# Optimization experiments

Hardware: AMD Instinct MI355X
Metric: run time of the kernel (lower is better)

The kernel has to match this reference:

```python
import jax, jax.numpy as jnp
import numpy as np

S, B, DIM = 1024, 4, 768
N_EXPERTS = 8
# hidden_dim = 256 * ceil(int(2*4*dim/3)/256) = 2048 for dim=768
HID = 2048


def setup_inputs() -> dict:
    key = jax.random.key(0)
    ks = jax.random.split(key, 6)
    scale = 0.02
    return {
        "hidden_states": jax.random.normal(ks[0], (S, B, DIM), dtype=jnp.float32),
        "router_w": jax.random.normal(ks[1], (DIM, N_EXPERTS), dtype=jnp.float32) * scale,
        "router_b": jnp.zeros((N_EXPERTS,), dtype=jnp.float32),
        "w1": jax.random.normal(ks[2], (N_EXPERTS, DIM, HID), dtype=jnp.float32) * scale,
        "w2": jax.random.normal(ks[3], (N_EXPERTS, DIM, HID), dtype=jnp.float32) * scale,
        "w3": jax.random.normal(ks[4], (N_EXPERTS, HID, DIM), dtype=jnp.float32) * scale,
    }


def reference(hidden_states, router_w, router_b, w1, w2, w3):
    s, b, h = hidden_states.shape
    # top-1 router
    route = jax.nn.softmax(hidden_states @ router_w + router_b, axis=2)  # [s,b,E]
    max_prob = jnp.max(route, axis=2).reshape(-1, 1)   # [T,1]
    max_ind = jnp.argmax(route, axis=2).reshape(-1)    # [T]
    x = hidden_states.reshape(-1, h)                   # [T,d]

    out = jnp.zeros_like(x)
    # fixed small loop over experts; masked dispatch (tokens not routed to e
    # are zeroed so they contribute nothing)
    for e in range(N_EXPERTS):
        mask = (max_ind == e)[:, None]                 # [T,1]
        xe = jnp.where(mask, x, 0.0)
        oe = (jax.nn.silu(xe @ w1[e]) * (xe @ w2[e])) @ w3[e]
        out = out + jnp.where(mask, oe, 0.0)

    # original stores expert outputs in a bf16 buffer before the prob combine
    out = out.astype(jnp.bfloat16) * max_prob          # bf16 * f32 -> f32
    return out.reshape(s, b, h)
```

## Files before the change

kernel.cpp:

```cpp
#include <hip/hip_runtime.h>


#define T_TOK 4096
#define DIM   768
#define HID   2048
#define NE    8
#define ECAP  1024

#define KB1 24
#define NB1 128
#define KB2 64
#define NB2 48
#define MBC 64

typedef _Float16 f16x8 __attribute__((ext_vector_type(8)));
typedef float    f32x4 __attribute__((ext_vector_type(4)));

#define AS1 __attribute__((address_space(1)))
#define AS3 __attribute__((address_space(3)))

__device__ __forceinline__ void gload_lds16(const _Float16* g, _Float16* l) {
    __builtin_amdgcn_global_load_lds((const AS1 unsigned int*)g,
                                     (AS3 unsigned int*)l, 16, 0, 0);
}

__device__ __forceinline__ float bf16_rne(float v) {
    unsigned u = __float_as_uint(v);
    unsigned r = (u + 0x7fffu + ((u >> 16) & 1u)) & 0xffff0000u;
    return __uint_as_float(r);
}

__global__ __launch_bounds__(256) void moe_convert_kernel(
    const float* __restrict__ w1, const float* __restrict__ w2,
    const float* __restrict__ w3, _Float16* __restrict__ w1s,
    _Float16* __restrict__ w2s, _Float16* __restrict__ w3s)
{
    const int bid = blockIdx.x;
    const float* src; _Float16* dst; int N, KBc, ngrp, kgrp;
    if (bid < 1536) {
        const int e = bid / 192, tile = bid % 192;
        src = w1 + (size_t)e * DIM * HID; dst = w1s + (size_t)e * NB1 * KB1 * 512;
        N = HID; KBc = KB1; ngrp = tile & 15; kgrp = tile >> 4;
    } else if (bid < 3072) {
        const int r = bid - 1536, e = r / 192, tile = r % 192;
        src = w2 + (size_t)e * DIM * HID; dst = w2s + (size_t)e * NB1 * KB1 * 512;
        N = HID; KBc = KB1; ngrp = tile & 15; kgrp = tile >> 4;
    } else {
        const int r = bid - 3072, e = r / 192, tile = r % 192;
        src = w3 + (size_t)e * HID * DIM; dst = w3s + (size_t)e * NB2 * KB2 * 512;
        N = DIM; KBc = KB2; ngrp = tile % 6; kgrp = tile / 6;
    }

    __shared__ float Lt[64 * 130];
    const int t  = threadIdx.x;
    const int c4 = (t & 31) * 4;
    const int r0 = (t >> 5) * 8;
    const float* p = src + (size_t)(kgrp * 64 + r0) * N + ngrp * 128 + c4;
    float4 v[8];
#pragma unroll
    for (int j = 0; j < 8; ++j) v[j] = *(const float4*)(p + (size_t)j * N);
#pragma unroll
    for (int j = 0; j < 8; ++j) {
        float* row = &Lt[(r0 + j) * 130 + c4];
        *(float2*)(row)     = make_float2(v[j].x, v[j].y);
        *(float2*)(row + 2) = make_float2(v[j].z, v[j].w);
    }
    __syncthreads();

    const int l = t & 63, w = t >> 6;
    const int fr = l & 15, fq = l >> 4;
#pragma unroll
    for (int i = 0; i < 4; ++i) {
        const int cell = w * 4 + i;
        const int kbl = cell >> 3, nbl = cell & 7;
        f16x8 h;
#pragma unroll
        for (int j = 0; j < 8; ++j)
            h[j] = (_Float16)Lt[(kbl * 32 + fq * 8 + j) * 130 + nbl * 16 + fr];
        const int nb = ngrp * 8 + nbl, kb = kgrp * 2 + kbl;
        *(f16x8*)(dst + ((size_t)nb * KBc + kb) * 512 + l * 8) = h;
    }
}

__global__ __launch_bounds__(256) void moe_router_kernel(
    const float* __restrict__ X, const float* __restrict__ rw,
    const float* __restrict__ rb, float* __restrict__ probs,
    int* __restrict__ maxind)
{
    const int t = blockIdx.x * 4 + (threadIdx.x >> 6);
    const int l = threadIdx.x & 63;
    const int e = l >> 3;
    const int g = l & 7;
    const float* x = X + (size_t)t * DIM + g * 96;
    const float* w = rw + e;

    double s0 = 0.0, s1 = 0.0;
#pragma unroll
    for (int j4 = 0; j4 < 24; ++j4) {
        const float4 xv = *(const float4*)(x + j4 * 4);
        const int d = (g * 96 + j4 * 4) * NE;
        s0 += (double)xv.x * (double)w[d];
        s1 += (double)xv.y * (double)w[d + NE];
        s0 += (double)xv.z * (double)w[d + 2 * NE];
        s1 += (double)xv.w * (double)w[d + 3 * NE];
    }
    double s = s0 + s1;
    s += __shfl_xor(s, 1, 64);
    s += __shfl_xor(s, 2, 64);
    s += __shfl_xor(s, 4, 64);
    s += (double)rb[e];

    double m = s; int mi = e;
#pragma unroll
    for (int o = 8; o <= 32; o <<= 1) {
        const double om = __shfl_xor(m, o, 64);
        const int   omi = __shfl_xor(mi, o, 64);
        if (om > m || (om == m && omi < mi)) { m = om; mi = omi; }
    }
    float ex = __expf((float)(s - m));
#pragma unroll
    for (int o = 8; o <= 32; o <<= 1) ex += __shfl_xor(ex, o, 64);

    if (l == 0) { probs[t] = 1.0f / ex; maxind[t] = mi; }
}

__global__ __launch_bounds__(256) void moe_lists_kernel(
    const int* __restrict__ maxind, int* __restrict__ counts,
    int* __restrict__ lists)
{
    const int e = blockIdx.x;
    const int tid = threadIdx.x, wid = tid >> 6, lane = tid & 63;
    __shared__ int wsum[4];
    int* dst = lists + e * T_TOK;
    int base = 0;
    for (int t0 = 0; t0 < T_TOK; t0 += 256) {
        const int t = t0 + tid;
        const bool pred = (maxind[t] == e);
        const unsigned long long bal = __ballot(pred);
        const int prefix = __popcll(bal & ((1ull << lane) - 1ull));
        if (lane == 0) wsum[wid] = __popcll(bal);
        __syncthreads();
        int woff = 0;
#pragma unroll
        for (int w2 = 0; w2 < 4; ++w2)
            if (w2 < wid) woff += wsum[w2];
        const int tot = wsum[0] + wsum[1] + wsum[2] + wsum[3];
        if (pred) dst[base + woff + prefix] = t;
        base += tot;
        __syncthreads();
    }
    if (tid == 0) counts[e] = base;
}

__global__ __launch_bounds__(256) void moe_gather_kernel(
    const float* __restrict__ X, const int* __restrict__ lists,
    const int* __restrict__ counts, _Float16* __restrict__ Ag)
{
    const int e = blockIdx.z;
    int cnt = counts[e]; if (cnt > ECAP) cnt = ECAP;
    const int mgrp = blockIdx.y;
    if (mgrp * 64 >= ((cnt + 63) & ~63)) return;
    const int t = threadIdx.x, w = t >> 6, l = t & 63;
    const int mb = mgrp * 4 + w;
    const int m  = mb * 16 + (l & 15);
    const bool valid = (m < cnt);
    const int tok = valid ? lists[e * T_TOK + m] : 0;
    const float* xr = X + (size_t)tok * DIM + (l >> 4) * 8;
#pragma unroll
    for (int i = 0; i < 4; ++i) {
        const int kb = blockIdx.x * 4 + i;
        float4 a = make_float4(0.f, 0.f, 0.f, 0.f), b = a;
        if (valid) {
            a = *(const float4*)(xr + kb * 32);
            b = *(const float4*)(xr + kb * 32 + 4);
        }
        f16x8 h;
        h[0] = (_Float16)a.x; h[1] = (_Float16)a.y; h[2] = (_Float16)a.z; h[3] = (_Float16)a.w;
        h[4] = (_Float16)b.x; h[5] = (_Float16)b.y; h[6] = (_Float16)b.z; h[7] = (_Float16)b.w;
        *(f16x8*)(Ag + ((size_t)(e * MBC + mb) * KB1 + kb) * 512 + l * 8) = h;
    }
}

__global__ __launch_bounds__(256, 4) void moe_gemm1_kernel(
    const _Float16* __restrict__ Ag, const _Float16* __restrict__ w1s,
    const _Float16* __restrict__ w2s, const int* __restrict__ counts,
    _Float16* __restrict__ Hs)
{
    const int e = blockIdx.z;
    int cnt = counts[e]; if (cnt > ECAP) cnt = ECAP;
    const int by = blockIdx.y, bx = blockIdx.x;
    if (by * 128 >= cnt) return;
    const int t = threadIdx.x, w = t >> 6, l = t & 63;
    const int wm = w & 1, wn = w >> 1;

    __shared__ _Float16 Ls[2][16 * 512];

    const int c0s = w * 4;
    const _Float16* gsrc[4];
#pragma unroll
    for (int i = 0; i < 4; ++i) {
        const int c = c0s + i;
        if (c < 8)
            gsrc[i] = Ag  + ((size_t)((e * MBC + by * 8 + c) * KB1)) * 512;
        else if (c < 12)
            gsrc[i] = w1s + ((size_t)((e * NB1 + bx * 4 + (c - 8)) * KB1)) * 512;
        else
            gsrc[i] = w2s + ((size_t)((e * NB1 + bx * 4 + (c - 12)) * KB1)) * 512;
        gsrc[i] += (size_t)l * 8;
    }

    f32x4 acc1[4][2], acc2[4][2];
    const f32x4 zero = {0.f, 0.f, 0.f, 0.f};
#pragma unroll
    for (int i = 0; i < 4; ++i)
#pragma unroll
        for (int j = 0; j < 2; ++j) { acc1[i][j] = zero; acc2[i][j] = zero; }

    auto STAGE = [&](int kb, _Float16* Lb) {
#pragma unroll
        for (int i = 0; i < 4; ++i)
            gload_lds16(gsrc[i] + (size_t)kb * 512, Lb + (c0s + i) * 512);
    };

    STAGE(0, &Ls[0][0]);
    __syncthreads();
    for (int kb = 0; kb < KB1; ++kb) {
        _Float16* Lb = &Ls[kb & 1][0];
        if (kb + 1 < KB1) STAGE(kb + 1, &Ls[(kb + 1) & 1][0]);

        f16x8 a[4], p[2], q[2];
#pragma unroll
        for (int i = 0; i < 4; ++i)
            a[i] = *(const f16x8*)(Lb + (wm * 4 + i) * 512 + l * 8);
#pragma unroll
        for (int j = 0; j < 2; ++j) {
            p[j] = *(const f16x8*)(Lb + (8  + wn * 2 + j) * 512 + l * 8);
            q[j] = *(const f16x8*)(Lb + (12 + wn * 2 + j) * 512 + l * 8);
        }
#pragma unroll
        for (int i = 0; i < 4; ++i)
#pragma unroll
            for (int j = 0; j < 2; ++j) {
                acc1[i][j] = __builtin_amdgcn_mfma_f32_16x16x32_f16(a[i], p[j], acc1[i][j], 0, 0, 0);
                acc2[i][j] = __builtin_amdgcn_mfma_f32_16x16x32_f16(a[i], q[j], acc2[i][j], 0, 0, 0);
            }
        __syncthreads();
    }

    _Float16* Ep = &Ls[0][0] + (size_t)w * (64 * 40);
    const int fq = l >> 4, fr = l & 15;
#pragma unroll
    for (int i = 0; i < 4; ++i)
#pragma unroll
        for (int j = 0; j < 2; ++j)
#pragma unroll
            for (int r = 0; r < 4; ++r) {
                const float h1 = acc1[i][j][r], h2 = acc2[i][j][r];
                const float s  = h1 / (1.f + __expf(-h1)) * h2;
                Ep[(i * 16 + fq * 4 + r) * 40 + j * 16 + fr] = (_Float16)s;
            }
    __syncthreads();
    const int kbH = bx * 2 + wn;
#pragma unroll
    for (int i = 0; i < 4; ++i) {
        f16x8 v = *(const f16x8*)&Ep[(i * 16 + fr) * 40 + fq * 8];
        *(f16x8*)(Hs + ((size_t)((e * MBC + by * 8 + wm * 4 + i) * KB2 + kbH)) * 512 + l * 8) = v;
    }
}

__global__ __launch_bounds__(256, 4) void moe_gemm2_kernel(
    const _Float16* __restrict__ Hs, const _Float16* __restrict__ w3s,
    const int* __restrict__ lists, const int* __restrict__ counts,
    const float* __restrict__ probs, float* __restrict__ out)
{
    const int e = blockIdx.z;
    int cnt = counts[e]; if (cnt > ECAP) cnt = ECAP;
    const int by = blockIdx.y, bx = blockIdx.x;
    if (by * 64 >= cnt) return;
    const int t = threadIdx.x, w = t >> 6, l = t & 63;

    __shared__ _Float16 La[2][8 * 512];

    const _Float16* Asrc = Hs + ((size_t)((e * MBC + by * 4 + w) * KB2)) * 512 + l * 8;
    const int nb0 = e * NB2 + bx * 8 + w * 2;
    const _Float16* Bb = w3s + ((size_t)nb0 * KB2) * 512 + l * 8;

    f32x4 acc[4][2];
    const f32x4 zero = {0.f, 0.f, 0.f, 0.f};
#pragma unroll
    for (int i = 0; i < 4; ++i) { acc[i][0] = zero; acc[i][1] = zero; }

    f16x8 vB0[4], vB1[4];

    auto STAGE_A = [&](int s, _Float16* Lb) {
        gload_lds16(Asrc + (size_t)(2 * s)     * 512, Lb +      w  * 512);
        gload_lds16(Asrc + (size_t)(2 * s + 1) * 512, Lb + (4 + w) * 512);
    };
    auto GB = [&](f16x8* vB, int s) {
#pragma unroll
        for (int u = 0; u < 2; ++u)
#pragma unroll
            for (int j = 0; j < 2; ++j)
                vB[u * 2 + j] = *(const f16x8*)(Bb + ((size_t)(j * KB2 + 2 * s + u)) * 512);
    };
    auto STEP = [&](int s, const f16x8* curB, f16x8* nxtB,
                    _Float16* Lb, _Float16* Ln) {
        if (s + 1 < KB2 / 2) { STAGE_A(s + 1, Ln); GB(nxtB, s + 1); }
#pragma unroll
        for (int u = 0; u < 2; ++u) {
            f16x8 a[4];
#pragma unroll
            for (int i = 0; i < 4; ++i)
                a[i] = *(const f16x8*)(Lb + (u * 4 + i) * 512 + l * 8);
#pragma unroll
            for (int i = 0; i < 4; ++i)
#pragma unroll
                for (int j = 0; j < 2; ++j)
                    acc[i][j] = __builtin_amdgcn_mfma_f32_16x16x32_f16(a[i], curB[u * 2 + j], acc[i][j], 0, 0, 0);
        }
        __syncthreads();
    };

    STAGE_A(0, &La[0][0]); GB(vB0, 0);
    __syncthreads();
    for (int s2 = 0; s2 < KB2 / 2; s2 += 2) {
        STEP(s2,     vB0, vB1, &La[0][0], &La[1][0]);
        STEP(s2 + 1, vB1, vB0, &La[1][0], &La[0][0]);
    }

    const int* list = lists + e * T_TOK;
    const int fq = l >> 4, fr = l & 15;
    const int c0 = bx * 128 + w * 32;
#pragma unroll
    for (int i = 0; i < 4; ++i)
#pragma unroll
        for (int r = 0; r < 4; ++r) {
            const int m = by * 64 + i * 16 + fq * 4 + r;
            if (m < cnt) {
                const int tok = list[m];
                const float pb = probs[tok];
                float* orow = out + (size_t)tok * DIM + c0 + fr;
                orow[0]  = bf16_rne(acc[i][0][r]) * pb;
                orow[16] = bf16_rne(acc[i][1][r]) * pb;
            }
        }
}

extern "C" void kernel_launch(void* const* d_in, const int* in_sizes, int n_in,
                              void* d_out, int out_size, void* d_ws, size_t ws_size,
                              hipStream_t stream) {
    const float* X  = (const float*)d_in[0];
    const float* rw = (const float*)d_in[1];
    const float* rb = (const float*)d_in[2];
    const float* w1 = (const float*)d_in[3];
    const float* w2 = (const float*)d_in[4];
    const float* w3 = (const float*)d_in[5];
    float* out = (float*)d_out;

    char* ws = (char*)d_ws;
    int*      counts = (int*)(ws + 0);
    int*      lists  = (int*)(ws + 256);
    float*    probs  = (float*)(ws + 131328);
    const size_t WSZ = 25165824;
    _Float16* w1s = (_Float16*)(ws + 147712);
    _Float16* w2s = (_Float16*)(ws + 147712 + WSZ);
    _Float16* w3s = (_Float16*)(ws + 147712 + 2 * WSZ);
    _Float16* Ag  = (_Float16*)(ws + 147712 + 3 * WSZ);
    _Float16* Hs  = (_Float16*)(ws + 147712 + 3 * WSZ + 12582912);
    int* maxind = (int*)Ag;

    hipLaunchKernelGGL(moe_convert_kernel, dim3(4608), dim3(256), 0, stream,
                       w1, w2, w3, w1s, w2s, w3s);
    hipLaunchKernelGGL(moe_router_kernel, dim3(T_TOK / 4), dim3(256), 0, stream,
                       X, rw, rb, probs, maxind);
    hipLaunchKernelGGL(moe_lists_kernel, dim3(NE), dim3(256), 0, stream,
                       maxind, counts, lists);
    hipLaunchKernelGGL(moe_gather_kernel, dim3(6, 16, 8), dim3(256), 0, stream,
                       X, lists, counts, Ag);
    hipLaunchKernelGGL(moe_gemm1_kernel, dim3(32, 8, 8), dim3(256), 0, stream,
                       Ag, w1s, w2s, counts, Hs);
    hipLaunchKernelGGL(moe_gemm2_kernel, dim3(6, 16, 8), dim3(256), 0, stream,
                       Hs, w3s, lists, counts, probs, out);
}
```

Baseline: 302.6 us.

## Fuse router and weight conversion into one kernel, build expert lists with atomics

Merges the router and the weight-conversion kernels into a single launch, with the first 1024 blocks doing routing and the rest converting weights. The separate list-building kernel is replaced by atomicAdd on per-expert counters, and a tiny init kernel zeroes the counters. This cuts launch count and the serial 8-block list pass. In exchange, tokens within each expert list are no longer in index order, which changes the gather order and memory locality.

```diff
diff --git a/kernel.cpp b/kernel.cpp
--- a/kernel.cpp
+++ b/kernel.cpp
@@ -30,23 +30,75 @@
     return __uint_as_float(r);
 }
 
-__global__ __launch_bounds__(256) void moe_convert_kernel(
+__global__ void moe_init_kernel(int* __restrict__ counts) {
+    if (threadIdx.x < NE) counts[threadIdx.x] = 0;
+}
+
+__global__ __launch_bounds__(256) void moe_front_kernel(
     const float* __restrict__ w1, const float* __restrict__ w2,
     const float* __restrict__ w3, _Float16* __restrict__ w1s,
-    _Float16* __restrict__ w2s, _Float16* __restrict__ w3s)
+    _Float16* __restrict__ w2s, _Float16* __restrict__ w3s,
+    const float* __restrict__ X, const float* __restrict__ rw,
+    const float* __restrict__ rb, float* __restrict__ probs,
+    int* __restrict__ counts, int* __restrict__ lists)
 {
     const int bid = blockIdx.x;
+
+    if (bid < 1024) {
+        const int t = bid * 4 + (threadIdx.x >> 6);
+        const int l = threadIdx.x & 63;
+        const int e = l >> 3;
+        const int g = l & 7;
+        const float* x = X + (size_t)t * DIM + g * 96;
+        const float* w = rw + e;
+
+        double s0 = 0.0, s1 = 0.0;
+#pragma unroll
+        for (int j4 = 0; j4 < 24; ++j4) {
+            const float4 xv = *(const float4*)(x + j4 * 4);
+            const int d = (g * 96 + j4 * 4) * NE;
+            s0 += (double)xv.x * (double)w[d];
+            s1 += (double)xv.y * (double)w[d + NE];
+            s0 += (double)xv.z * (double)w[d + 2 * NE];
+            s1 += (double)xv.w * (double)w[d + 3 * NE];
+        }
+        double s = s0 + s1;
+        s += __shfl_xor(s, 1, 64);
+        s += __shfl_xor(s, 2, 64);
+        s += __shfl_xor(s, 4, 64);
+        s += (double)rb[e];
+
+        double m = s; int mi = e;
+#pragma unroll
+        for (int o = 8; o <= 32; o <<= 1) {
+            const double om = __shfl_xor(m, o, 64);
+            const int   omi = __shfl_xor(mi, o, 64);
+            if (om > m || (om == m && omi < mi)) { m = om; mi = omi; }
+        }
+        float ex = __expf((float)(s - m));
+#pragma unroll
+        for (int o = 8; o <= 32; o <<= 1) ex += __shfl_xor(ex, o, 64);
+
+        if (l == 0) {
+            probs[t] = 1.0f / ex;
+            const int pos = atomicAdd(&counts[mi], 1);
+            if (pos < T_TOK) lists[mi * T_TOK + pos] = t;
+        }
+        return;
+    }
+
+    const int cb = bid - 1024;
     const float* src; _Float16* dst; int N, KBc, ngrp, kgrp;
-    if (bid < 1536) {
-        const int e = bid / 192, tile = bid % 192;
+    if (cb < 1536) {
+        const int e = cb / 192, tile = cb % 192;
         src = w1 + (size_t)e * DIM * HID; dst = w1s + (size_t)e * NB1 * KB1 * 512;
         N = HID; KBc = KB1; ngrp = tile & 15; kgrp = tile >> 4;
-    } else if (bid < 3072) {
-        const int r = bid - 1536, e = r / 192, tile = r % 192;
+    } else if (cb < 3072) {
+        const int r = cb - 1536, e = r / 192, tile = r % 192;
         src = w2 + (size_t)e * DIM * HID; dst = w2s + (size_t)e * NB1 * KB1 * 512;
         N = HID; KBc = KB1; ngrp = tile & 15; kgrp = tile >> 4;
     } else {
-        const int r = bid - 3072, e = r / 192, tile = r % 192;
+        const int r = cb - 3072, e = r / 192, tile = r % 192;
         src = w3 + (size_t)e * HID * DIM; dst = w3s + (size_t)e * NB2 * KB2 * 512;
         N = DIM; KBc = KB2; ngrp = tile % 6; kgrp = tile / 6;
     }
@@ -80,76 +132,6 @@
         const int nb = ngrp * 8 + nbl, kb = kgrp * 2 + kbl;
         *(f16x8*)(dst + ((size_t)nb * KBc + kb) * 512 + l * 8) = h;
     }
-}
-
-__global__ __launch_bounds__(256) void moe_router_kernel(
-    const float* __restrict__ X, const float* __restrict__ rw,
-    const float* __restrict__ rb, float* __restrict__ probs,
-    int* __restrict__ maxind)
-{
-    const int t = blockIdx.x * 4 + (threadIdx.x >> 6);
-    const int l = threadIdx.x & 63;
-    const int e = l >> 3;
-    const int g = l & 7;
-    const float* x = X + (size_t)t * DIM + g * 96;
-    const float* w = rw + e;
-
-    double s0 = 0.0, s1 = 0.0;
-#pragma unroll
-    for (int j4 = 0; j4 < 24; ++j4) {
-        const float4 xv = *(const float4*)(x + j4 * 4);
-        const int d = (g * 96 + j4 * 4) * NE;
-        s0 += (double)xv.x * (double)w[d];
-        s1 += (double)xv.y * (double)w[d + NE];
-        s0 += (double)xv.z * (double)w[d + 2 * NE];
-        s1 += (double)xv.w * (double)w[d + 3 * NE];
-    }
-    double s = s0 + s1;
-    s += __shfl_xor(s, 1, 64);
-    s += __shfl_xor(s, 2, 64);
-    s += __shfl_xor(s, 4, 64);
-    s += (double)rb[e];
-
-    double m = s; int mi = e;
-#pragma unroll
-    for (int o = 8; o <= 32; o <<= 1) {
-        const double om = __shfl_xor(m, o, 64);
-        const int   omi = __shfl_xor(mi, o, 64);
-        if (om > m || (om == m && omi < mi)) { m = om; mi = omi; }
-    }
-    float ex = __expf((float)(s - m));
-#pragma unroll
-    for (int o = 8; o <= 32; o <<= 1) ex += __shfl_xor(ex, o, 64);
-
-    if (l == 0) { probs[t] = 1.0f / ex; maxind[t] = mi; }
-}
-
-__global__ __launch_bounds__(256) void moe_lists_kernel(
-    const int* __restrict__ maxind, int* __restrict__ counts,
-    int* __restrict__ lists)
-{
-    const int e = blockIdx.x;
-    const int tid = threadIdx.x, wid = tid >> 6, lane = tid & 63;
-    __shared__ int wsum[4];
-    int* dst = lists + e * T_TOK;
-    int base = 0;
-    for (int t0 = 0; t0 < T_TOK; t0 += 256) {
-        const int t = t0 + tid;
-        const bool pred = (maxind[t] == e);
-        const unsigned long long bal = __ballot(pred);
-        const int prefix = __popcll(bal & ((1ull << lane) - 1ull));
-        if (lane == 0) wsum[wid] = __popcll(bal);
-        __syncthreads();
-        int woff = 0;
-#pragma unroll
-        for (int w2 = 0; w2 < 4; ++w2)
-            if (w2 < wid) woff += wsum[w2];
-        const int tot = wsum[0] + wsum[1] + wsum[2] + wsum[3];
-        if (pred) dst[base + woff + prefix] = t;
-        base += tot;
-        __syncthreads();
-    }
-    if (tid == 0) counts[e] = base;
 }
 
 __global__ __launch_bounds__(256) void moe_gather_kernel(
@@ -367,14 +349,10 @@
     _Float16* w3s = (_Float16*)(ws + 147712 + 2 * WSZ);
     _Float16* Ag  = (_Float16*)(ws + 147712 + 3 * WSZ);
     _Float16* Hs  = (_Float16*)(ws + 147712 + 3 * WSZ + 12582912);
-    int* maxind = (int*)Ag;
-
-    hipLaunchKernelGGL(moe_convert_kernel, dim3(4608), dim3(256), 0, stream,
-                       w1, w2, w3, w1s, w2s, w3s);
-    hipLaunchKernelGGL(moe_router_kernel, dim3(T_TOK / 4), dim3(256), 0, stream,
-                       X, rw, rb, probs, maxind);
-    hipLaunchKernelGGL(moe_lists_kernel, dim3(NE), dim3(256), 0, stream,
-                       maxind, counts, lists);
+
+    hipLaunchKernelGGL(moe_init_kernel, dim3(1), dim3(64), 0, stream, counts);
+    hipLaunchKernelGGL(moe_front_kernel, dim3(5632), dim3(256), 0, stream,
+                       w1, w2, w3, w1s, w2s, w3s, X, rw, rb, probs, counts, lists);
     hipLaunchKernelGGL(moe_gather_kernel, dim3(6, 16, 8), dim3(256), 0, stream,
                        X, lists, counts, Ag);
     hipLaunchKernelGGL(moe_gemm1_kernel, dim3(32, 8, 8), dim3(256), 0, stream,
```

Result: slower. 317.9 us (+5.1%).
